# Performance work log

Measured on AMD Instinct MI355X. Metric: run time of the kernel, lower is better.

Reference implementation:

```python
import jax, jax.numpy as jnp
import numpy as np

NS, NV = 128, 64        # multiplicities of 0e and 1o node irreps
TPC = NS + NV           # 192: tp-out channels for each of 0e and 1o
N_NODES, N_EDGES, NUM_BASIS = 16000, 256000, 16
INV_SQRT3 = 1.0 / np.sqrt(3.0).astype(np.float32)


def setup_inputs() -> dict:
    key = jax.random.key(0)
    ks = jax.random.split(key, 12)
    return {
        "node_feat": jax.random.normal(ks[0], (N_NODES, NS + 3 * NV), jnp.float32),
        "edge_attr": jax.random.normal(ks[1], (N_EDGES, NUM_BASIS), jnp.float32),
        "edge_rshs": jax.random.normal(ks[2], (N_EDGES, 4), jnp.float32),
        "edge_index": jax.random.randint(ks[3], (2, N_EDGES), 0, N_NODES, jnp.int64 if jax.config.jax_enable_x64 else jnp.int32),
        "W_pre_s": jax.random.normal(ks[4], (NS, NS), jnp.float32),
        "b_pre_s": jnp.zeros((NS,), jnp.float32),
        "W_pre_v": jax.random.normal(ks[5], (NV, NV), jnp.float32),
        "W1": jax.random.normal(ks[6], (NUM_BASIS, 128), jnp.float32),
        "b1": jnp.zeros((128,), jnp.float32),
        "W2": jax.random.normal(ks[7], (128, 2 * (NS + NV)), jnp.float32),
        "b2": jnp.zeros((2 * (NS + NV),), jnp.float32),
        "W_post_s": jax.random.normal(ks[8], (TPC, NS), jnp.float32),
        "W_post_v": jax.random.normal(ks[9], (TPC, NV), jnp.float32),
    }


def reference(node_feat, edge_attr, edge_rshs, edge_index,
              W_pre_s, b_pre_s, W_pre_v, W1, b1, W2, b2, W_post_s, W_post_v):
    n = node_feat.shape[0]
    s = node_feat[:, :NS]                       # [N,128] scalars (0e)
    v = node_feat[:, NS:].reshape(n, NV, 3)     # [N,64,3] vectors (1o)

    # lin_node_pre (irrep-wise linear, bias on scalars only, fan-in normalized)
    x_s = s @ W_pre_s * (1.0 / np.sqrt(NS)) + b_pre_s
    x_v = jnp.einsum("nuc,uv->nvc", v, W_pre_v) * (1.0 / np.sqrt(NV))

    dst, src = edge_index[0], edge_index[1]
    s_j = x_s[src]                              # gather [E,128]
    v_j = x_v[src]                              # gather [E,64,3]
    r0 = edge_rshs[:, :1]                       # [E,1]  0e sph-harm
    r1 = edge_rshs[:, 1:4]                      # [E,3]  1o sph-harm

    # per-edge TP weights from radial MLP: 16 -> 128 -> silu -> 384
    h = jax.nn.silu(edge_attr @ W1 + b1)
    w = h @ W2 + b2                             # [E,384]
    w_ss0 = w[:, :NS]                           # (0e x 0e -> 0e), 128
    w_vv0 = w[:, NS:NS + NV]                    # (1o x 1o -> 0e), 64
    w_sv1 = w[:, NS + NV:2 * NS + NV]           # (0e x 1o -> 1o), 128
    w_vs1 = w[:, 2 * NS + NV:]                  # (1o x 0e -> 1o), 64

    # uvu tensor product (CG: 1 for l=0 couplings, 1/sqrt(3) for 1x1->0)
    msg_s = jnp.concatenate([
        w_ss0 * s_j * r0,                                        # [E,128]
        w_vv0 * jnp.einsum("euc,ec->eu", v_j, r1) * INV_SQRT3,   # [E,64]
    ], axis=-1)                                                  # [E,192]
    msg_v = jnp.concatenate([
        (w_sv1 * s_j)[:, :, None] * r1[:, None, :],              # [E,128,3]
        w_vs1[:, :, None] * v_j * r0[:, :, None],                # [E,64,3]
    ], axis=1)                                                   # [E,192,3]

    # scatter-reduce messages to destination nodes
    acc_s = jax.ops.segment_sum(msg_s, dst, num_segments=n)      # [N,192]
    acc_v = jax.ops.segment_sum(msg_v, dst, num_segments=n)      # [N,192,3]

    # gate activation: silu on scalars, norm-sigmoid gating on vectors
    g_s = jax.nn.silu(acc_s)
    v_norm = jnp.sqrt(jnp.sum(acc_v * acc_v, axis=-1) + 1e-12)   # [N,192]
    g_v = acc_v * jax.nn.sigmoid(v_norm)[:, :, None]

    # lin_node_post back to node irreps
    p_s = g_s @ W_post_s * (1.0 / np.sqrt(TPC))
    p_v = jnp.einsum("nuc,uv->nvc", g_v, W_post_v) * (1.0 / np.sqrt(TPC))

    out_s = x_s + p_s
    out_v = x_v + p_v
    return jnp.concatenate([out_s, out_v.reshape(n, NV * 3)], axis=-1)
```

## Files before the change

### kernel.cpp

```cpp
#include <hip/hip_runtime.h>
#include <hip/hip_bf16.h>

#define NS 128
#define NV 64
#define TPC 192
#define NBASIS 16
#define HID 128
#define WOUT 384
#define NNODE 16000
#define NEDGE 256000
#define EPB 32
#define GVPLANE 3072000
#define VPLANE  1024000

typedef __attribute__((ext_vector_type(8))) short bf16x8;
typedef __attribute__((ext_vector_type(8))) unsigned short u16x8;
typedef __attribute__((ext_vector_type(4))) unsigned short u16x4;
typedef __attribute__((ext_vector_type(4))) float f32x4;

__device__ __forceinline__ float silu_f(float x) { return x / (1.0f + __expf(-x)); }
__device__ __forceinline__ unsigned short bf16b(float x) {
  __hip_bfloat16 h = __float2bfloat16(x);
  return *reinterpret_cast<unsigned short*>(&h);
}
__device__ __forceinline__ float bf2f(unsigned short u) {
  return __uint_as_float(((unsigned)u) << 16);
}

__global__ __launch_bounds__(256) void pack_weights(
    const float* __restrict__ W1, const float* __restrict__ W2,
    const float* __restrict__ Wqs, const float* __restrict__ Wqv,
    const float* __restrict__ Wps, const float* __restrict__ Wpv,
    unsigned short* __restrict__ W1P, unsigned short* __restrict__ W2P,
    unsigned short* __restrict__ WqsP, unsigned short* __restrict__ WqvP,
    unsigned short* __restrict__ WpsP, unsigned short* __restrict__ WpvP,
    int* __restrict__ cursor) {
  const int id = blockIdx.x * 256 + threadIdx.x;
  const int j = id & 7, lane = (id >> 3) & 63;
  const int kj = (lane >> 4) * 8 + j;
  const int nc = lane & 15;
  const float SC = 0.07216878364870323f;
  if (id < NNODE) cursor[id] = 0;
  if (id < 24 * 4 * 64 * 8) {
    const int kc = (id >> 9) & 3, nt = id >> 11;
    W2P[id] = bf16b(W2[(kc * 32 + kj) * WOUT + nt * 16 + nc]);
  }
  if (id < 8 * 64 * 8) {
    const int nt = id >> 9;
    W1P[id] = (kj < NBASIS) ? bf16b(W1[kj * HID + nt * 16 + nc]) : (unsigned short)0;
  }
  if (id < 8 * 6 * 64 * 8) {
    const int kc = (id >> 9) % 6, nt = id / (6 * 512);
    WqsP[id] = bf16b(Wqs[(kc * 32 + kj) * NS + nt * 16 + nc] * SC);
  }
  if (id < 4 * 6 * 64 * 8) {
    const int kc = (id >> 9) % 6, nt = id / (6 * 512);
    WqvP[id] = bf16b(Wqv[(kc * 32 + kj) * NV + nt * 16 + nc] * SC);
  }
  if (id < 8 * 4 * 64 * 8) {
    const int kc = (id >> 9) & 3, nt = id >> 11;
    WpsP[id] = bf16b(Wps[(kc * 32 + kj) * NS + nt * 16 + nc] * 0.08838834764831845f);
  }
  if (id < 4 * 2 * 64 * 8) {
    const int kc = (id >> 9) & 1, nt = id >> 10;
    WpvP[id] = bf16b(Wpv[(kc * 32 + kj) * NV + nt * 16 + nc] * 0.125f);
  }
}

__global__ __launch_bounds__(256) void node_pre_mfma(
    const float* __restrict__ node_feat, const float* __restrict__ bps,
    const unsigned short* __restrict__ WpsP, const unsigned short* __restrict__ WpvP,
    float* __restrict__ x_s, float* __restrict__ x_v,
    unsigned short* __restrict__ x_s16, unsigned short* __restrict__ xv16) {
  __shared__ __align__(16) unsigned short as_[32 * 136];
  __shared__ __align__(16) unsigned short avp[3][32 * 72];
  const int n0 = blockIdx.x * 32;
  const int t = threadIdx.x;
  const int lane = t & 63;
  const int w = t >> 6;
  const int l15 = lane & 15;
  const int l4 = lane >> 4;

  #pragma unroll
  for (int p = 0; p < 4; ++p) {
    const int idx = p * 256 + t;
    const int r = idx >> 5, c4 = idx & 31;
    const float4 v = *(const float4*)&node_feat[(size_t)(n0 + r) * 320 + c4 * 4];
    u16x4 tmp;
    tmp[0] = bf16b(v.x); tmp[1] = bf16b(v.y); tmp[2] = bf16b(v.z); tmp[3] = bf16b(v.w);
    *(u16x4*)&as_[r * 136 + c4 * 4] = tmp;
  }
  #pragma unroll
  for (int p = 0; p < 8; ++p) {
    const int idx = p * 256 + t;
    const int r = idx >> 6, u = idx & 63;
    const float* vp = &node_feat[(size_t)(n0 + r) * 320 + 128 + u * 3];
    avp[0][r * 72 + u] = bf16b(vp[0]);
    avp[1][r * 72 + u] = bf16b(vp[1]);
    avp[2][r * 72 + u] = bf16b(vp[2]);
  }
  __syncthreads();

  f32x4 accS[2][2];
  #pragma unroll
  for (int jj = 0; jj < 2; ++jj) {
    const float b = bps[(w * 2 + jj) * 16 + l15];
    #pragma unroll
    for (int mt = 0; mt < 2; ++mt) accS[jj][mt] = (f32x4){b, b, b, b};
  }
  f32x4 accV[3][2];
  #pragma unroll
  for (int c = 0; c < 3; ++c)
    #pragma unroll
    for (int mt = 0; mt < 2; ++mt) accV[c][mt] = (f32x4){0.f, 0.f, 0.f, 0.f};

  #pragma unroll
  for (int kc = 0; kc < 4; ++kc) {
    bf16x8 aS[2];
    #pragma unroll
    for (int mt = 0; mt < 2; ++mt)
      aS[mt] = *(const bf16x8*)&as_[(mt * 16 + l15) * 136 + kc * 32 + l4 * 8];
    const bf16x8 bS0 = *(const bf16x8*)&WpsP[(((size_t)(w * 2 + 0) * 4 + kc) * 64 + lane) * 8];
    const bf16x8 bS1 = *(const bf16x8*)&WpsP[(((size_t)(w * 2 + 1) * 4 + kc) * 64 + lane) * 8];
    #pragma unroll
    for (int mt = 0; mt < 2; ++mt) {
      accS[0][mt] = __builtin_amdgcn_mfma_f32_16x16x32_bf16(aS[mt], bS0, accS[0][mt], 0, 0, 0);
      accS[1][mt] = __builtin_amdgcn_mfma_f32_16x16x32_bf16(aS[mt], bS1, accS[1][mt], 0, 0, 0);
    }
  }
  #pragma unroll
  for (int kc = 0; kc < 2; ++kc) {
    const bf16x8 bV = *(const bf16x8*)&WpvP[(((size_t)w * 2 + kc) * 64 + lane) * 8];
    #pragma unroll
    for (int c = 0; c < 3; ++c) {
      bf16x8 aV[2];
      #pragma unroll
      for (int mt = 0; mt < 2; ++mt)
        aV[mt] = *(const bf16x8*)&avp[c][(mt * 16 + l15) * 72 + kc * 32 + l4 * 8];
      #pragma unroll
      for (int mt = 0; mt < 2; ++mt)
        accV[c][mt] = __builtin_amdgcn_mfma_f32_16x16x32_bf16(aV[mt], bV, accV[c][mt], 0, 0, 0);
    }
  }

  #pragma unroll
  for (int jj = 0; jj < 2; ++jj) {
    const int col = (w * 2 + jj) * 16 + l15;
    #pragma unroll
    for (int mt = 0; mt < 2; ++mt)
      #pragma unroll
      for (int i = 0; i < 4; ++i) {
        const int row = n0 + mt * 16 + l4 * 4 + i;
        const float r = accS[jj][mt][i];
        x_s[(size_t)row * NS + col] = r;
        x_s16[(size_t)row * NS + col] = bf16b(r);
      }
  }
  {
    const int vch = w * 16 + l15;
    #pragma unroll
    for (int mt = 0; mt < 2; ++mt)
      #pragma unroll
      for (int i = 0; i < 4; ++i) {
        const int row = n0 + mt * 16 + l4 * 4 + i;
        const float r0 = accV[0][mt][i], r1 = accV[1][mt][i], r2 = accV[2][mt][i];
        float* xp = x_v + (size_t)row * (NV * 3) + vch * 3;
        xp[0] = r0; xp[1] = r1; xp[2] = r2;
        xv16[(size_t)0 * VPLANE + (size_t)row * NV + vch] = bf16b(r0);
        xv16[(size_t)1 * VPLANE + (size_t)row * NV + vch] = bf16b(r1);
        xv16[(size_t)2 * VPLANE + (size_t)row * NV + vch] = bf16b(r2);
      }
  }
}

__global__ void hist_kernel(const int* __restrict__ ei, int* __restrict__ cnt) {
  int e = blockIdx.x * 256 + threadIdx.x;
  if (e < NEDGE) atomicAdd(&cnt[ei[e]], 1);
}

__global__ __launch_bounds__(256) void scan_kernel(
    const int* __restrict__ cnt, int* __restrict__ row_start, int* __restrict__ cursor) {
  __shared__ int part[256];
  const int t = threadIdx.x;
  const int base = t * 63;
  int s = 0;
  for (int i = 0; i < 63; ++i) {
    int idx = base + i;
    if (idx < NNODE) s += cnt[idx];
  }
  part[t] = s;
  __syncthreads();
  if (t == 0) {
    int run = 0;
    for (int i = 0; i < 256; ++i) { int x = part[i]; part[i] = run; run += x; }
  }
  __syncthreads();
  int run = part[t];
  for (int i = 0; i < 63; ++i) {
    int idx = base + i;
    if (idx < NNODE) {
      int c = cnt[idx];
      row_start[idx] = run;
      cursor[idx] = run;
      run += c;
    }
  }
  if (t == 255) row_start[NNODE] = run;
}

__global__ void scatter_kernel(const int* __restrict__ ei,
                               const float* __restrict__ edge_rshs,
                               int* __restrict__ cursor, int* __restrict__ perm,
                               float4* __restrict__ meta) {
  int e = blockIdx.x * 256 + threadIdx.x;
  if (e < NEDGE) {
    int p = atomicAdd(&cursor[ei[e]], 1);
    perm[e] = p;
    float4 m;
    m.x = __int_as_float(ei[NEDGE + e]);
    m.y = edge_rshs[e * 4 + 1];
    m.z = edge_rshs[e * 4 + 2];
    m.w = edge_rshs[e * 4 + 3];
    meta[p] = m;
  }
}

__global__ __launch_bounds__(256) void edge_mlp_mfma(
    const float* __restrict__ edge_attr, const float* __restrict__ edge_rshs,
    const int* __restrict__ edge_index, const int* __restrict__ perm,
    const unsigned short* __restrict__ W1P, const float* __restrict__ b1,
    const unsigned short* __restrict__ W2P, const float* __restrict__ b2,
    const unsigned short* __restrict__ x_s16, const unsigned short* __restrict__ xv16,
    unsigned short* __restrict__ msg) {
  union SMU {
    struct { unsigned short ea[32 * 48]; unsigned short Hs[32 * 136]; } p1;
    unsigned short msgb[32 * 392];
  };
  __shared__ __align__(16) SMU sm;
  __shared__ __align__(16) unsigned short sj[32][136];
  __shared__ __align__(16) unsigned short vd[32][72];
  __shared__ unsigned short b2s[384];
  __shared__ unsigned short b1s[128];
  __shared__ int src_sh[32];
  __shared__ int slot_sh[32];
  __shared__ float rsh_sh[32][4];
  const int t = threadIdx.x;
  const int lane = t & 63;
  const int w = t >> 6;
  const int l15 = lane & 15;
  const int l4 = lane >> 4;
  const int eblk = blockIdx.x * EPB;

  if (t < 32 * 4) rsh_sh[t >> 2][t & 3] = edge_rshs[(size_t)eblk * 4 + t];
  if (t < 32) {
    src_sh[t] = edge_index[NEDGE + eblk + t];
    slot_sh[t] = perm[eblk + t];
  }
  for (int i = t; i < 384; i += 256) b2s[i] = bf16b(b2[i]);
  if (t < 128) b1s[t] = bf16b(b1[t]);
  if (t < 128) {
    const int e = t >> 2, q = t & 3;
    const float4 v = *(const float4*)&edge_attr[(size_t)(eblk + e) * NBASIS + q * 4];
    u16x4 tmp;
    tmp[0] = bf16b(v.x); tmp[1] = bf16b(v.y); tmp[2] = bf16b(v.z); tmp[3] = bf16b(v.w);
    *(u16x4*)&sm.p1.ea[e * 48 + q * 4] = tmp;
  } else {
    const int idx = t - 128;
    const int e = idx >> 2, q = idx & 3;
    *(u16x8*)&sm.p1.ea[e * 48 + 16 + q * 8] = (u16x8){0, 0, 0, 0, 0, 0, 0, 0};
  }
  __syncthreads();

  {
    const int mt = w & 1, ch = w >> 1;
    const bf16x8 afrag = *(const bf16x8*)&sm.p1.ea[(mt * 16 + l15) * 48 + l4 * 8];
    #pragma unroll
    for (int nt = 0; nt < 4; ++nt) {
      const int ntg = ch * 4 + nt;
      const bf16x8 bfrag = *(const bf16x8*)&W1P[((size_t)ntg * 64 + lane) * 8];
      const int col = ntg * 16 + l15;
      const float bias = bf2f(b1s[col]);
      f32x4 d = {bias, bias, bias, bias};
      d = __builtin_amdgcn_mfma_f32_16x16x32_bf16(afrag, bfrag, d, 0, 0, 0);
      #pragma unroll
      for (int i = 0; i < 4; ++i) {
        const int e = mt * 16 + l4 * 4 + i;
        sm.p1.Hs[e * 136 + col] = bf16b(silu_f(d[i]));
      }
    }
  }
  #pragma unroll
  for (int p = 0; p < 2; ++p) {
    const int idx = p * 256 + t;
    const int e = idx >> 4, c8 = idx & 15;
    *(u16x8*)&sj[e][c8 * 8] =
        *(const u16x8*)&x_s16[(size_t)src_sh[e] * NS + c8 * 8];
  }
  #pragma unroll
  for (int p = 0; p < 8; ++p) {
    const int idx = p * 256 + t;
    const int e = idx >> 6, u = idx & 63;
    const size_t base = (size_t)src_sh[e] * NV + u;
    const float v0 = bf2f(xv16[base]);
    const float v1 = bf2f(xv16[VPLANE + base]);
    const float v2 = bf2f(xv16[2 * VPLANE + base]);
    const float dotv = fmaf(v0, rsh_sh[e][1], fmaf(v1, rsh_sh[e][2], v2 * rsh_sh[e][3]));
    vd[e][u] = bf16b(dotv * 0.5773502691896258f);
  }
  __syncthreads();

  bf16x8 afr[2][4];
  #pragma unroll
  for (int mt = 0; mt < 2; ++mt)
    #pragma unroll
    for (int k = 0; k < 4; ++k)
      afr[mt][k] = *(const bf16x8*)&sm.p1.Hs[(mt * 16 + l15) * 136 + k * 32 + l4 * 8];

  float r0a[2][4];
  #pragma unroll
  for (int mt = 0; mt < 2; ++mt)
    #pragma unroll
    for (int i = 0; i < 4; ++i) r0a[mt][i] = rsh_sh[mt * 16 + l4 * 4 + i][0];
  __syncthreads();

  #pragma unroll
  for (int nn = 0; nn < 6; ++nn) {
    const int nt = w * 6 + nn;
    bf16x8 bfr[4];
    #pragma unroll
    for (int k = 0; k < 4; ++k)
      bfr[k] = *(const bf16x8*)&W2P[(((size_t)nt * 4 + k) * 64 + lane) * 8];
    const int col = nt * 16 + l15;
    const float bias = bf2f(b2s[col]);
    f32x4 acc0 = {bias, bias, bias, bias}, acc1 = {bias, bias, bias, bias};
    #pragma unroll
    for (int k = 0; k < 4; ++k) {
      acc0 = __builtin_amdgcn_mfma_f32_16x16x32_bf16(afr[0][k], bfr[k], acc0, 0, 0, 0);
      acc1 = __builtin_amdgcn_mfma_f32_16x16x32_bf16(afr[1][k], bfr[k], acc1, 0, 0, 0);
    }
    if (col < NS) {
      #pragma unroll
      for (int mt = 0; mt < 2; ++mt)
        #pragma unroll
        for (int i = 0; i < 4; ++i) {
          const int e = mt * 16 + l4 * 4 + i;
          const float wv = mt ? acc1[i] : acc0[i];
          sm.msgb[e * 392 + col] = bf16b(wv * bf2f(sj[e][col]) * r0a[mt][i]);
        }
    } else if (col < NS + NV) {
      const int u = col - NS;
      #pragma unroll
      for (int mt = 0; mt < 2; ++mt)
        #pragma unroll
        for (int i = 0; i < 4; ++i) {
          const int e = mt * 16 + l4 * 4 + i;
          const float wv = mt ? acc1[i] : acc0[i];
          sm.msgb[e * 392 + col] = bf16b(wv * bf2f(vd[e][u]));
        }
    } else if (col < 2 * NS + NV) {
      const int sjc = col - (NS + NV);
      #pragma unroll
      for (int mt = 0; mt < 2; ++mt)
        #pragma unroll
        for (int i = 0; i < 4; ++i) {
          const int e = mt * 16 + l4 * 4 + i;
          const float wv = mt ? acc1[i] : acc0[i];
          sm.msgb[e * 392 + col] = bf16b(wv * bf2f(sj[e][sjc]));
        }
    } else {
      #pragma unroll
      for (int mt = 0; mt < 2; ++mt)
        #pragma unroll
        for (int i = 0; i < 4; ++i) {
          const int e = mt * 16 + l4 * 4 + i;
          const float wv = mt ? acc1[i] : acc0[i];
          sm.msgb[e * 392 + col] = bf16b(wv * r0a[mt][i]);
        }
    }
  }
  __syncthreads();

  #pragma unroll
  for (int p = 0; p < 6; ++p) {
    const int idx = p * 256 + t;
    const int e = idx / 48, c = idx - e * 48;
    const u16x8 vv = *(const u16x8*)&sm.msgb[e * 392 + c * 8];
    *(u16x8*)&msg[(size_t)slot_sh[e] * 384 + c * 8] = vv;
  }
}

__global__ __launch_bounds__(256) void node_gather(
    const unsigned short* __restrict__ msg, const int* __restrict__ row_start,
    const float4* __restrict__ meta, const unsigned short* __restrict__ xv16,
    unsigned short* __restrict__ gs16, unsigned short* __restrict__ gv16) {
  const int n = blockIdx.x;
  const int t = threadIdx.x;
  const int role = t >> 6, ln = t & 63;
  const int beg = row_start[n], end = row_start[n + 1];

  float a0 = 0.f, a1 = 0.f, a2 = 0.f;

  if (role == 0) {
    const unsigned short* mp = msg + (size_t)beg * 384;
    int i = beg;
    for (; i + 8 <= end; i += 8, mp += 3072) {
      unsigned int pr[8]; unsigned short v2[8];
      #pragma unroll
      for (int u = 0; u < 8; ++u) {
        pr[u] = *(const unsigned int*)(mp + u * 384 + 2 * ln);
        v2[u] = mp[u * 384 + 128 + ln];
      }
      #pragma unroll
      for (int u = 0; u < 8; ++u) {
        a0 += __uint_as_float(pr[u] << 16);
        a1 += __uint_as_float(pr[u] & 0xffff0000u);
        a2 += bf2f(v2[u]);
      }
    }
    for (; i < end; ++i, mp += 384) {
      const unsigned int p = *(const unsigned int*)(mp + 2 * ln);
      a0 += __uint_as_float(p << 16);
      a1 += __uint_as_float(p & 0xffff0000u);
      a2 += bf2f(mp[128 + ln]);
    }
    gs16[(size_t)n * 192 + 2 * ln]     = bf16b(silu_f(a0));
    gs16[(size_t)n * 192 + 2 * ln + 1] = bf16b(silu_f(a1));
    gs16[(size_t)n * 192 + 128 + ln]   = bf16b(silu_f(a2));
  } else {
    if (role < 3) {
      const unsigned short* mp = msg + (size_t)beg * 384 + 192 + (role - 1) * 64 + ln;
      int i = beg;
      for (; i + 8 <= end; i += 8, mp += 3072) {
        float4 mt[8]; unsigned short v[8];
        #pragma unroll
        for (int u = 0; u < 8; ++u) { mt[u] = meta[i + u]; v[u] = mp[u * 384]; }
        #pragma unroll
        for (int u = 0; u < 8; ++u) {
          const float m = bf2f(v[u]);
          a0 = fmaf(m, mt[u].y, a0);
          a1 = fmaf(m, mt[u].z, a1);
          a2 = fmaf(m, mt[u].w, a2);
        }
      }
      for (; i < end; ++i, mp += 384) {
        const float4 mt = meta[i];
        const float m = bf2f(mp[0]);
        a0 = fmaf(m, mt.y, a0); a1 = fmaf(m, mt.z, a1); a2 = fmaf(m, mt.w, a2);
      }
    } else {
      const unsigned short* mp = msg + (size_t)beg * 384 + 320 + ln;
      int i = beg;
      for (; i + 8 <= end; i += 8, mp += 3072) {
        float4 mt[8]; unsigned short v[8];
        #pragma unroll
        for (int u = 0; u < 8; ++u) { mt[u] = meta[i + u]; v[u] = mp[u * 384]; }
        unsigned short x0[8], x1[8], x2[8];
        #pragma unroll
        for (int u = 0; u < 8; ++u) {
          const size_t base = (size_t)__float_as_int(mt[u].x) * NV + ln;
          x0[u] = xv16[base]; x1[u] = xv16[VPLANE + base]; x2[u] = xv16[2 * VPLANE + base];
        }
        #pragma unroll
        for (int u = 0; u < 8; ++u) {
          const float m = bf2f(v[u]);
          a0 = fmaf(m, bf2f(x0[u]), a0);
          a1 = fmaf(m, bf2f(x1[u]), a1);
          a2 = fmaf(m, bf2f(x2[u]), a2);
        }
      }
      for (; i < end; ++i, mp += 384) {
        const float4 mt = meta[i];
        const float m = bf2f(mp[0]);
        const size_t base = (size_t)__float_as_int(mt.x) * NV + ln;
        a0 = fmaf(m, bf2f(xv16[base]), a0);
        a1 = fmaf(m, bf2f(xv16[VPLANE + base]), a1);
        a2 = fmaf(m, bf2f(xv16[2 * VPLANE + base]), a2);
      }
    }
    const float nrm = sqrtf(fmaf(a0, a0, fmaf(a1, a1, a2 * a2)) + 1e-12f);
    const float sg = 1.f / (1.f + __expf(-nrm));
    const int u = (role < 3) ? (role - 1) * 64 + ln : 128 + ln;
    gv16[(size_t)0 * GVPLANE + (size_t)n * 192 + u] = bf16b(a0 * sg);
    gv16[(size_t)1 * GVPLANE + (size_t)n * 192 + u] = bf16b(a1 * sg);
    gv16[(size_t)2 * GVPLANE + (size_t)n * 192 + u] = bf16b(a2 * sg);
  }
}

__global__ __launch_bounds__(256) void node_post_mfma(
    const unsigned short* __restrict__ gs16, const unsigned short* __restrict__ gv16,
    const unsigned short* __restrict__ WqsP, const unsigned short* __restrict__ WqvP,
    const float* __restrict__ x_s, const float* __restrict__ x_v,
    float* __restrict__ out) {
  __shared__ __align__(16) unsigned short gsA[32 * 200];
  __shared__ __align__(16) unsigned short gvA[3][32 * 200];
  const int n0 = blockIdx.x * 32;
  const int t = threadIdx.x;
  const int lane = t & 63;
  const int w = t >> 6;
  const int l15 = lane & 15;
  const int l4 = lane >> 4;

  {
    const unsigned short* sp = gs16 + (size_t)n0 * 192;
    for (int idx = t; idx < 768; idx += 256) {
      const int row = idx / 24, ch = idx - row * 24;
      *(u16x8*)&gsA[row * 200 + ch * 8] = *(const u16x8*)&sp[row * 192 + ch * 8];
    }
    #pragma unroll
    for (int c = 0; c < 3; ++c) {
      const unsigned short* vp = gv16 + (size_t)c * GVPLANE + (size_t)n0 * 192;
      for (int idx = t; idx < 768; idx += 256) {
        const int row = idx / 24, ch = idx - row * 24;
        *(u16x8*)&gvA[c][row * 200 + ch * 8] = *(const u16x8*)&vp[row * 192 + ch * 8];
      }
    }
  }
  __syncthreads();

  f32x4 accS[2][2];
  f32x4 accV[3][2];
  #pragma unroll
  for (int j = 0; j < 2; ++j)
    #pragma unroll
    for (int mt = 0; mt < 2; ++mt) accS[j][mt] = (f32x4){0.f, 0.f, 0.f, 0.f};
  #pragma unroll
  for (int c = 0; c < 3; ++c)
    #pragma unroll
    for (int mt = 0; mt < 2; ++mt) accV[c][mt] = (f32x4){0.f, 0.f, 0.f, 0.f};

  #pragma unroll
  for (int kc = 0; kc < 6; ++kc) {
    bf16x8 aS[2], aV[3][2];
    #pragma unroll
    for (int mt = 0; mt < 2; ++mt)
      aS[mt] = *(const bf16x8*)&gsA[(mt * 16 + l15) * 200 + kc * 32 + l4 * 8];
    #pragma unroll
    for (int c = 0; c < 3; ++c)
      #pragma unroll
      for (int mt = 0; mt < 2; ++mt)
        aV[c][mt] = *(const bf16x8*)&gvA[c][(mt * 16 + l15) * 200 + kc * 32 + l4 * 8];
    const bf16x8 bS0 = *(const bf16x8*)&WqsP[(((size_t)(w * 2 + 0) * 6 + kc) * 64 + lane) * 8];
    const bf16x8 bS1 = *(const bf16x8*)&WqsP[(((size_t)(w * 2 + 1) * 6 + kc) * 64 + lane) * 8];
    const bf16x8 bV  = *(const bf16x8*)&WqvP[(((size_t)w * 6 + kc) * 64 + lane) * 8];
    #pragma unroll
    for (int mt = 0; mt < 2; ++mt) {
      accS[0][mt] = __builtin_amdgcn_mfma_f32_16x16x32_bf16(aS[mt], bS0, accS[0][mt], 0, 0, 0);
      accS[1][mt] = __builtin_amdgcn_mfma_f32_16x16x32_bf16(aS[mt], bS1, accS[1][mt], 0, 0, 0);
    }
    #pragma unroll
    for (int c = 0; c < 3; ++c)
      #pragma unroll
      for (int mt = 0; mt < 2; ++mt)
        accV[c][mt] = __builtin_amdgcn_mfma_f32_16x16x32_bf16(aV[c][mt], bV, accV[c][mt], 0, 0, 0);
  }

  #pragma unroll
  for (int j = 0; j < 2; ++j) {
    const int col = (w * 2 + j) * 16 + l15;
    #pragma unroll
    for (int mt = 0; mt < 2; ++mt)
      #pragma unroll
      for (int i = 0; i < 4; ++i) {
        const int row = n0 + mt * 16 + l4 * 4 + i;
        out[(size_t)row * 320 + col] =
            x_s[(size_t)row * NS + col] + accS[j][mt][i];
      }
  }
  {
    const int vch = w * 16 + l15;
    #pragma unroll
    for (int mt = 0; mt < 2; ++mt)
      #pragma unroll
      for (int i = 0; i < 4; ++i) {
        const int row = n0 + mt * 16 + l4 * 4 + i;
        const float* xvp = x_v + (size_t)row * (NV * 3) + vch * 3;
        float o0 = xvp[0] + accV[0][mt][i];
        float o1 = xvp[1] + accV[1][mt][i];
        float o2 = xvp[2] + accV[2][mt][i];
        float* op = out + (size_t)row * 320 + NS + vch * 3;
        op[0] = o0; op[1] = o1; op[2] = o2;
      }
  }
}

extern "C" void kernel_launch(void* const* d_in, const int* in_sizes, int n_in,
                              void* d_out, int out_size, void* d_ws, size_t ws_size,
                              hipStream_t stream) {
  const float* node_feat = (const float*)d_in[0];
  const float* edge_attr = (const float*)d_in[1];
  const float* edge_rshs = (const float*)d_in[2];
  const int*   edge_index = (const int*)d_in[3];
  const float* Wps = (const float*)d_in[4];
  const float* bps = (const float*)d_in[5];
  const float* Wpv = (const float*)d_in[6];
  const float* W1  = (const float*)d_in[7];
  const float* b1  = (const float*)d_in[8];
  const float* W2  = (const float*)d_in[9];
  const float* b2  = (const float*)d_in[10];
  const float* Wqs = (const float*)d_in[11];
  const float* Wqv = (const float*)d_in[12];
  float* out = (float*)d_out;

  float* x_s = (float*)d_ws;
  float* x_v = x_s + (size_t)NNODE * NS;
  unsigned short* msg = (unsigned short*)(x_v + (size_t)NNODE * NV * 3);
  unsigned short* W1P = msg + (size_t)NEDGE * 384;
  unsigned short* W2P = W1P + 8 * 64 * 8;
  unsigned short* WqsP = W2P + 24 * 4 * 64 * 8;
  unsigned short* WqvP = WqsP + 8 * 6 * 64 * 8;
  unsigned short* WpsP = WqvP + 4 * 6 * 64 * 8;
  unsigned short* WpvP = WpsP + 8 * 4 * 64 * 8;
  unsigned short* x_s16 = WpvP + 4 * 2 * 64 * 8;
  unsigned short* xv16 = x_s16 + (size_t)NNODE * NS;
  unsigned short* gs16 = xv16 + (size_t)3 * VPLANE;
  unsigned short* gv16 = gs16 + (size_t)NNODE * 192;
  float4* meta = (float4*)(gv16 + (size_t)3 * GVPLANE);
  int* row_start = (int*)(meta + NEDGE);
  int* cursor = row_start + (NNODE + 1);
  int* perm = cursor + NNODE;

  pack_weights<<<192, 256, 0, stream>>>(W1, W2, Wqs, Wqv, Wps, Wpv,
      W1P, W2P, WqsP, WqvP, WpsP, WpvP, cursor);
  node_pre_mfma<<<NNODE / 32, 256, 0, stream>>>(node_feat, bps, WpsP, WpvP,
      x_s, x_v, x_s16, xv16);
  hist_kernel<<<(NEDGE + 255) / 256, 256, 0, stream>>>(edge_index, cursor);
  scan_kernel<<<1, 256, 0, stream>>>(cursor, row_start, cursor);
  scatter_kernel<<<(NEDGE + 255) / 256, 256, 0, stream>>>(edge_index, edge_rshs,
      cursor, perm, meta);
  edge_mlp_mfma<<<NEDGE / EPB, 256, 0, stream>>>(edge_attr, edge_rshs, edge_index,
      perm, W1P, b1, W2P, b2, x_s16, xv16, msg);
  node_gather<<<NNODE, 256, 0, stream>>>(msg, row_start, meta, xv16, gs16, gv16);
  node_post_mfma<<<NNODE / 32, 256, 0, stream>>>(gs16, gv16, WqsP, WqvP,
      x_s, x_v, out);
}
```

Baseline: 252.1 us.

## Fuse histogram into node_pre and slot assignment into edge MLP kernel

Folds the destination-degree histogram into the node_pre kernel using a grid-stride loop, and moves the CSR slot atomic and the meta write into the edge MLP kernel, which removes the separate hist and scatter launches and the perm buffer. The node gather loops also gain a 16-wide unrolled path to raise memory-level parallelism. The trade-offs are extra tail work in node_pre, atomics on the critical path of the edge kernel, and higher register pressure in the gather kernel.

```diff
diff --git a/kernel.cpp b/kernel.cpp
--- a/kernel.cpp
+++ b/kernel.cpp
@@ -70,6 +70,7 @@
 __global__ __launch_bounds__(256) void node_pre_mfma(
     const float* __restrict__ node_feat, const float* __restrict__ bps,
     const unsigned short* __restrict__ WpsP, const unsigned short* __restrict__ WpvP,
+    const int* __restrict__ edge_index, int* __restrict__ cnt,
     float* __restrict__ x_s, float* __restrict__ x_v,
     unsigned short* __restrict__ x_s16, unsigned short* __restrict__ xv16) {
   __shared__ __align__(16) unsigned short as_[32 * 136];
@@ -171,11 +172,9 @@
         xv16[(size_t)2 * VPLANE + (size_t)row * NV + vch] = bf16b(r2);
       }
   }
-}
-
-__global__ void hist_kernel(const int* __restrict__ ei, int* __restrict__ cnt) {
-  int e = blockIdx.x * 256 + threadIdx.x;
-  if (e < NEDGE) atomicAdd(&cnt[ei[e]], 1);
+
+  for (int e = blockIdx.x * 256 + t; e < NEDGE; e += gridDim.x * 256)
+    atomicAdd(&cnt[edge_index[e]], 1);
 }
 
 __global__ __launch_bounds__(256) void scan_kernel(
@@ -208,26 +207,10 @@
   if (t == 255) row_start[NNODE] = run;
 }
 
-__global__ void scatter_kernel(const int* __restrict__ ei,
-                               const float* __restrict__ edge_rshs,
-                               int* __restrict__ cursor, int* __restrict__ perm,
-                               float4* __restrict__ meta) {
-  int e = blockIdx.x * 256 + threadIdx.x;
-  if (e < NEDGE) {
-    int p = atomicAdd(&cursor[ei[e]], 1);
-    perm[e] = p;
-    float4 m;
-    m.x = __int_as_float(ei[NEDGE + e]);
-    m.y = edge_rshs[e * 4 + 1];
-    m.z = edge_rshs[e * 4 + 2];
-    m.w = edge_rshs[e * 4 + 3];
-    meta[p] = m;
-  }
-}
-
 __global__ __launch_bounds__(256) void edge_mlp_mfma(
     const float* __restrict__ edge_attr, const float* __restrict__ edge_rshs,
-    const int* __restrict__ edge_index, const int* __restrict__ perm,
+    const int* __restrict__ edge_index, int* __restrict__ cursor,
+    float4* __restrict__ meta,
     const unsigned short* __restrict__ W1P, const float* __restrict__ b1,
     const unsigned short* __restrict__ W2P, const float* __restrict__ b2,
     const unsigned short* __restrict__ x_s16, const unsigned short* __restrict__ xv16,
@@ -253,8 +236,9 @@
 
   if (t < 32 * 4) rsh_sh[t >> 2][t & 3] = edge_rshs[(size_t)eblk * 4 + t];
   if (t < 32) {
+    const int dst = edge_index[eblk + t];
+    slot_sh[t] = atomicAdd(&cursor[dst], 1);
     src_sh[t] = edge_index[NEDGE + eblk + t];
-    slot_sh[t] = perm[eblk + t];
   }
   for (int i = t; i < 384; i += 256) b2s[i] = bf16b(b2[i]);
   if (t < 128) b1s[t] = bf16b(b1[t]);
@@ -271,6 +255,13 @@
   }
   __syncthreads();
 
+  if (t < 32) {
+    float4 m;
+    m.x = __int_as_float(src_sh[t]);
+    m.y = rsh_sh[t][1]; m.z = rsh_sh[t][2]; m.w = rsh_sh[t][3];
+    meta[slot_sh[t]] = m;
+  }
+
   {
     const int mt = w & 1, ch = w >> 1;
     const bf16x8 afrag = *(const bf16x8*)&sm.p1.ea[(mt * 16 + l15) * 48 + l4 * 8];
@@ -403,6 +394,20 @@
   if (role == 0) {
     const unsigned short* mp = msg + (size_t)beg * 384;
     int i = beg;
+    for (; i + 16 <= end; i += 16, mp += 6144) {
+      unsigned int pr[16]; unsigned short v2[16];
+      #pragma unroll
+      for (int u = 0; u < 16; ++u) {
+        pr[u] = *(const unsigned int*)(mp + u * 384 + 2 * ln);
+        v2[u] = mp[u * 384 + 128 + ln];
+      }
+      #pragma unroll
+      for (int u = 0; u < 16; ++u) {
+        a0 += __uint_as_float(pr[u] << 16);
+        a1 += __uint_as_float(pr[u] & 0xffff0000u);
+        a2 += bf2f(v2[u]);
+      }
+    }
     for (; i + 8 <= end; i += 8, mp += 3072) {
       unsigned int pr[8]; unsigned short v2[8];
       #pragma unroll
@@ -430,6 +435,18 @@
     if (role < 3) {
       const unsigned short* mp = msg + (size_t)beg * 384 + 192 + (role - 1) * 64 + ln;
       int i = beg;
+      for (; i + 16 <= end; i += 16, mp += 6144) {
+        float4 mt[16]; unsigned short v[16];
+        #pragma unroll
+        for (int u = 0; u < 16; ++u) { mt[u] = meta[i + u]; v[u] = mp[u * 384]; }
+        #pragma unroll
+        for (int u = 0; u < 16; ++u) {
+          const float m = bf2f(v[u]);
+          a0 = fmaf(m, mt[u].y, a0);
+          a1 = fmaf(m, mt[u].z, a1);
+          a2 = fmaf(m, mt[u].w, a2);
+        }
+      }
       for (; i + 8 <= end; i += 8, mp += 3072) {
         float4 mt[8]; unsigned short v[8];
         #pragma unroll
@@ -617,18 +634,14 @@
   float4* meta = (float4*)(gv16 + (size_t)3 * GVPLANE);
   int* row_start = (int*)(meta + NEDGE);
   int* cursor = row_start + (NNODE + 1);
-  int* perm = cursor + NNODE;
 
   pack_weights<<<192, 256, 0, stream>>>(W1, W2, Wqs, Wqv, Wps, Wpv,
       W1P, W2P, WqsP, WqvP, WpsP, WpvP, cursor);
   node_pre_mfma<<<NNODE / 32, 256, 0, stream>>>(node_feat, bps, WpsP, WpvP,
-      x_s, x_v, x_s16, xv16);
-  hist_kernel<<<(NEDGE + 255) / 256, 256, 0, stream>>>(edge_index, cursor);
+      edge_index, cursor, x_s, x_v, x_s16, xv16);
   scan_kernel<<<1, 256, 0, stream>>>(cursor, row_start, cursor);
-  scatter_kernel<<<(NEDGE + 255) / 256, 256, 0, stream>>>(edge_index, edge_rshs,
-      cursor, perm, meta);
   edge_mlp_mfma<<<NEDGE / EPB, 256, 0, stream>>>(edge_attr, edge_rshs, edge_index,
-      perm, W1P, b1, W2P, b2, x_s16, xv16, msg);
+      cursor, meta, W1P, b1, W2P, b2, x_s16, xv16, msg);
   node_gather<<<NNODE, 256, 0, stream>>>(msg, row_start, meta, xv16, gs16, gv16);
   node_post_mfma<<<NNODE / 32, 256, 0, stream>>>(gs16, gv16, WqsP, WqvP,
       x_s, x_v, out);
```

After: 251.2 us. Within noise of the previous version (-0.4%).
